# Kernel tuning notes

Hardware: AMD Instinct MI355X
Metric: run time of the kernel (lower is better)

## Reference

```python
import jax, jax.numpy as jnp
import numpy as np

EXP_CLAMP = 1.0e6
DENOM_EPS = 1e-10
LRELU_ALPHA = 0.01


def setup_inputs() -> dict:
    key = jax.random.key(0)
    k1, k2, k3, k4, k5, k6 = jax.random.split(key, 6)
    B, N, E, F = 4, 16384, 262144, 64
    h = jax.random.normal(k1, (B, N, F), dtype=jnp.float32)
    edge = jax.random.randint(k2, (B, E, 2), 0, N, dtype=jnp.int32)
    edge_num = jax.random.randint(k3, (B,), 1, E, dtype=jnp.int32)
    edge_weight = jax.random.uniform(k4, (B, E), dtype=jnp.float32)
    W = jax.random.normal(k5, (F, F), dtype=jnp.float32) * 0.15  # xavier-ish scale
    a = jax.random.normal(k6, (1, 2 * F), dtype=jnp.float32) * 0.12
    return {"h": h, "edge": edge, "edge_num": edge_num,
            "edge_weight": edge_weight, "W": W, "a": a}


def _seg_sum(src, idx, num_segments):
    # src: [E, ...], idx: [E] -> [num_segments, ...]
    return jax.ops.segment_sum(src, idx, num_segments=num_segments)


def reference(h, edge, edge_num, edge_weight, W, a):
    B, N, Fin = h.shape
    E = edge.shape[1]
    # linear transform: Wh = h @ W^T  -> [B, N, Fout]
    Wh = jnp.einsum('bnf,of->bno', h, W)
    ctr = edge[:, :, 0]  # [B, E]
    nbr = edge[:, :, 1]  # [B, E]
    Wh_c = jnp.take_along_axis(Wh, ctr[:, :, None], axis=1)  # [B, E, Fout]
    Wh_n = jnp.take_along_axis(Wh, nbr[:, :, None], axis=1)  # [B, E, Fout]
    a_input = jnp.concatenate([Wh_c, Wh_n], axis=-1) * edge_weight[:, :, None]
    # attention logits: leakyrelu(a_input @ a^T), squeeze to [B, E]
    att1 = jax.nn.leaky_relu(jnp.einsum('bek,k->be', a_input, a[0]), LRELU_ALPHA)
    # per-batch valid-edge mask (edges beyond edge_num zeroed, as in torch loop)
    mask = (jnp.arange(E, dtype=jnp.int32)[None, :] < edge_num[:, None])
    x_exp = jnp.clip(jnp.exp(att1), 0.0, EXP_CLAMP) * mask.astype(att1.dtype)
    # segment softmax denominator over center nodes
    denom = DENOM_EPS + jax.vmap(_seg_sum, in_axes=(0, 0, None))(x_exp, ctr, N)  # [B, N]
    att = x_exp / jnp.take_along_axis(denom, ctr, axis=1)  # [B, E]
    # weighted neighbor aggregation via scatter-add on center index
    att_Wh = Wh_n * att[:, :, None]  # masked edges already have att == 0
    h_prime = jax.vmap(_seg_sum, in_axes=(0, 0, None))(att_Wh, ctr, N)  # [B, N, Fout]
    return jax.nn.relu(h_prime)
```

## Files before the change

kernel.cpp:

```cpp
#include <hip/hip_runtime.h>

#define BB 4
#define NN 16384
#define EE 262144
#define FF 64
#define ROWS (BB * NN)
#define CAP 64
#define CHUNKS 64
#define CHUNK_E (EE / CHUNKS)
#define TILE_R 256

typedef __bf16 bf16x8 __attribute__((ext_vector_type(8)));
typedef float  f32x4  __attribute__((ext_vector_type(4)));

__device__ __forceinline__ unsigned short f32_to_bf16(float f) {
    unsigned int u = __float_as_uint(f);
    u += 0x7FFFu + ((u >> 16) & 1u);
    return (unsigned short)(u >> 16);
}

__global__ __launch_bounds__(256) void mfma_kernel(
    const float* __restrict__ h, const float* __restrict__ W,
    const float* __restrict__ a,
    unsigned short* __restrict__ Wh,
    float* __restrict__ sc, float* __restrict__ sn)
{
    __shared__ float wc[FF], wn[FF];
    const int t = threadIdx.x;
    const int lane = t & 63;
    const int m = lane & 15;
    const int q = lane >> 4;

    if (t < 128) {
        const int f = t & 63;
        const float* av = a + (t >> 6) * FF;
        float s = 0.0f;
        #pragma unroll 8
        for (int o = 0; o < FF; ++o)
            s = fmaf(av[o], W[o * FF + f], s);
        (t < 64 ? wc : wn)[f] = s;
    }

    bf16x8 bfrag[4][2];
    #pragma unroll
    for (int nt = 0; nt < 4; ++nt) {
        const float* wr = W + (nt * 16 + m) * FF;
        #pragma unroll
        for (int kh = 0; kh < 2; ++kh) {
            const float4 v0 = *(const float4*)(wr + kh * 32 + q * 8);
            const float4 v1 = *(const float4*)(wr + kh * 32 + q * 8 + 4);
            bf16x8 b;
            b[0] = (__bf16)v0.x; b[1] = (__bf16)v0.y;
            b[2] = (__bf16)v0.z; b[3] = (__bf16)v0.w;
            b[4] = (__bf16)v1.x; b[5] = (__bf16)v1.y;
            b[6] = (__bf16)v1.z; b[7] = (__bf16)v1.w;
            bfrag[nt][kh] = b;
        }
    }

    __syncthreads();

    const int waveId = (blockIdx.x * 256 + t) >> 6;
    const int R0 = waveId * 16;
    const float* hr = h + (size_t)(R0 + m) * FF;
    bf16x8 af[2];
    float s1 = 0.0f, s2 = 0.0f;
    #pragma unroll
    for (int kh = 0; kh < 2; ++kh) {
        const float4 v0 = *(const float4*)(hr + kh * 32 + q * 8);
        const float4 v1 = *(const float4*)(hr + kh * 32 + q * 8 + 4);
        bf16x8 aa;
        aa[0] = (__bf16)v0.x; aa[1] = (__bf16)v0.y;
        aa[2] = (__bf16)v0.z; aa[3] = (__bf16)v0.w;
        aa[4] = (__bf16)v1.x; aa[5] = (__bf16)v1.y;
        aa[6] = (__bf16)v1.z; aa[7] = (__bf16)v1.w;
        af[kh] = aa;
        const int fb = kh * 32 + q * 8;
        const float4 c0 = *(const float4*)&wc[fb];
        const float4 c1 = *(const float4*)&wc[fb + 4];
        const float4 n0 = *(const float4*)&wn[fb];
        const float4 n1 = *(const float4*)&wn[fb + 4];
        s1 = fmaf(v0.x, c0.x, fmaf(v0.y, c0.y, fmaf(v0.z, c0.z, fmaf(v0.w, c0.w, s1))));
        s1 = fmaf(v1.x, c1.x, fmaf(v1.y, c1.y, fmaf(v1.z, c1.z, fmaf(v1.w, c1.w, s1))));
        s2 = fmaf(v0.x, n0.x, fmaf(v0.y, n0.y, fmaf(v0.z, n0.z, fmaf(v0.w, n0.w, s2))));
        s2 = fmaf(v1.x, n1.x, fmaf(v1.y, n1.y, fmaf(v1.z, n1.z, fmaf(v1.w, n1.w, s2))));
    }
    s1 += __shfl_xor(s1, 16); s2 += __shfl_xor(s2, 16);
    s1 += __shfl_xor(s1, 32); s2 += __shfl_xor(s2, 32);
    if (lane < 16) { sc[R0 + m] = s1; sn[R0 + m] = s2; }

    #pragma unroll
    for (int nt = 0; nt < 4; ++nt) {
        f32x4 acc = {0.f, 0.f, 0.f, 0.f};
        acc = __builtin_amdgcn_mfma_f32_16x16x32_bf16(af[0], bfrag[nt][0], acc, 0, 0, 0);
        acc = __builtin_amdgcn_mfma_f32_16x16x32_bf16(af[1], bfrag[nt][1], acc, 0, 0, 0);
        #pragma unroll
        for (int i = 0; i < 4; ++i)
            Wh[(size_t)(R0 + q * 4 + i) * FF + nt * 16 + m] = f32_to_bf16(acc[i]);
    }
}

__global__ __launch_bounds__(256) void hist_kernel(
    const int* __restrict__ edge, const int* __restrict__ edge_num,
    unsigned short* __restrict__ histG)
{
    __shared__ unsigned int hist[NN];
    const int g = blockIdx.x;
    const int b = g >> 6, c = g & (CHUNKS - 1);
    const int t = threadIdx.x;
    const int en = edge_num[b];
    const int e0 = c * CHUNK_E;
    if (e0 >= en) return;

    for (int r = t; r < NN; r += 256) hist[r] = 0u;
    __syncthreads();

    const int2* ep = (const int2*)edge + (size_t)b * EE + e0;
    const int nAct = min(en - e0, CHUNK_E);
    for (int j = t; j < nAct; j += 256)
        atomicAdd(&hist[ep[j].x], 1u);
    __syncthreads();

    ushort2* out2 = (ushort2*)(histG + (size_t)g * NN);
    for (int r2 = t; r2 < NN / 2; r2 += 256) {
        ushort2 v;
        v.x = (unsigned short)hist[2 * r2];
        v.y = (unsigned short)hist[2 * r2 + 1];
        out2[r2] = v;
    }
}

__global__ __launch_bounds__(256) void scan_kernel(
    const int* __restrict__ edge_num,
    unsigned short* __restrict__ histG, int* __restrict__ cnt)
{
    __shared__ unsigned short tile[CHUNKS][TILE_R];
    const int g = blockIdx.x;
    const int b = g >> 6, tl = g & 63;
    const int r0 = tl * TILE_R;
    const int t = threadIdx.x;
    const int en = edge_num[b];
    const int nact = min((en + CHUNK_E - 1) / CHUNK_E, CHUNKS);

    for (int c = 0; c < nact; ++c)
        tile[c][t] = histG[(size_t)(b * CHUNKS + c) * NN + r0 + t];
    __syncthreads();

    unsigned int acc = 0;
    for (int c = 0; c < nact; ++c) {
        const unsigned int v = tile[c][t];
        tile[c][t] = (unsigned short)(acc > 65535u ? 65535u : acc);
        acc += v;
    }
    cnt[b * NN + r0 + t] = (int)acc;

    for (int c = 0; c < nact; ++c)
        histG[(size_t)(b * CHUNKS + c) * NN + r0 + t] = tile[c][t];
}

__global__ __launch_bounds__(256) void scatter_kernel(
    const int* __restrict__ edge, const int* __restrict__ edge_num,
    const unsigned short* __restrict__ baseG,
    unsigned int* __restrict__ payload)
{
    __shared__ unsigned int slotA[NN];
    const int g = blockIdx.x;
    const int b = g >> 6, c = g & (CHUNKS - 1);
    const int t = threadIdx.x;
    const int en = edge_num[b];
    const int e0 = c * CHUNK_E;
    if (e0 >= en) return;

    const ushort2* b2 = (const ushort2*)(baseG + (size_t)(b * CHUNKS + c) * NN);
    for (int r2 = t; r2 < NN / 2; r2 += 256) {
        const ushort2 v = b2[r2];
        slotA[2 * r2]     = v.x;
        slotA[2 * r2 + 1] = v.y;
    }
    __syncthreads();

    const int2* ep = (const int2*)edge + (size_t)b * EE + e0;
    const int nAct = min(en - e0, CHUNK_E);
    unsigned int* payB = payload + (size_t)b * NN * CAP;

    for (int j = t; j < nAct; j += 256) {
        const int2 e2 = ep[j];
        const unsigned int slot = atomicAdd(&slotA[e2.x], 1u);
        const unsigned int eid  = (unsigned int)(e0 + j);
        if (slot < CAP)
            payB[(size_t)e2.x * CAP + slot] = (eid << 14) | (unsigned int)e2.y;
    }
}

__global__ __launch_bounds__(256) void gather_kernel(
    const int* __restrict__ cnt, const unsigned int* __restrict__ payload,
    const uint2* __restrict__ Wh2,
    const float* __restrict__ sc, const float* __restrict__ sn,
    const float* __restrict__ ew,
    float* __restrict__ out)
{
    const int bi = blockIdx.x;
    const int xcd = bi & 7;
    const int batch = xcd >> 1;
    const int within = ((bi >> 3) << 1) | (xcd & 1);
    const int rg = batch * 4096 + within;

    const int lane = threadIdx.x & 63;
    const int wave = threadIdx.x >> 6;
    const int row = rg * 4 + wave;
    const int grp = lane >> 4;
    const int gl  = lane & 15;
    const unsigned int* pl = payload + (size_t)row * CAP;
    const uint2* WhB = Wh2 + (size_t)batch * NN * 16;
    const float* snB = sn + batch * NN;
    const float* ewB = ew + (size_t)batch * EE;

    int deg = cnt[row];
    const unsigned int praw = pl[lane];
    const float scr = sc[row];
    if (deg > CAP) deg = CAP;

    const float s0 = ewB[praw >> 14] * (scr + snB[praw & 0x3FFFu]);
    const float s1 = s0 > 0.0f ? s0 : 0.01f * s0;
    const float xe = fminf(__expf(s1), 1000000.0f);
    const unsigned int p = (lane < deg)
        ? (((__float_as_uint(xe) + 0x2000u) & 0xFFFFC000u) | (praw & 0x3FFFu))
        : 0u;

    float a0 = 0.f, a1 = 0.f, a2 = 0.f, a3 = 0.f, dsum = 0.f;
    for (int jj = 0; jj < deg; jj += 16) {
        const unsigned int pv0 = __shfl(p, jj + grp);
        const unsigned int pv1 = __shfl(p, jj + grp + 4);
        const unsigned int pv2 = __shfl(p, jj + grp + 8);
        const unsigned int pv3 = __shfl(p, jj + grp + 12);
        const uint2 w0 = WhB[(size_t)(pv0 & 0x3FFFu) * 16 + gl];
        const uint2 w1 = WhB[(size_t)(pv1 & 0x3FFFu) * 16 + gl];
        const uint2 w2 = WhB[(size_t)(pv2 & 0x3FFFu) * 16 + gl];
        const uint2 w3 = WhB[(size_t)(pv3 & 0x3FFFu) * 16 + gl];
        const float xe0 = __uint_as_float(pv0 & 0xFFFFC000u);
        const float xe1 = __uint_as_float(pv1 & 0xFFFFC000u);
        const float xe2 = __uint_as_float(pv2 & 0xFFFFC000u);
        const float xe3 = __uint_as_float(pv3 & 0xFFFFC000u);
        a0 = fmaf(xe0, __uint_as_float(w0.x << 16),         a0);
        a1 = fmaf(xe0, __uint_as_float(w0.x & 0xFFFF0000u), a1);
        a2 = fmaf(xe0, __uint_as_float(w0.y << 16),         a2);
        a3 = fmaf(xe0, __uint_as_float(w0.y & 0xFFFF0000u), a3);
        a0 = fmaf(xe1, __uint_as_float(w1.x << 16),         a0);
        a1 = fmaf(xe1, __uint_as_float(w1.x & 0xFFFF0000u), a1);
        a2 = fmaf(xe1, __uint_as_float(w1.y << 16),         a2);
        a3 = fmaf(xe1, __uint_as_float(w1.y & 0xFFFF0000u), a3);
        a0 = fmaf(xe2, __uint_as_float(w2.x << 16),         a0);
        a1 = fmaf(xe2, __uint_as_float(w2.x & 0xFFFF0000u), a1);
        a2 = fmaf(xe2, __uint_as_float(w2.y << 16),         a2);
        a3 = fmaf(xe2, __uint_as_float(w2.y & 0xFFFF0000u), a3);
        a0 = fmaf(xe3, __uint_as_float(w3.x << 16),         a0);
        a1 = fmaf(xe3, __uint_as_float(w3.x & 0xFFFF0000u), a1);
        a2 = fmaf(xe3, __uint_as_float(w3.y << 16),         a2);
        a3 = fmaf(xe3, __uint_as_float(w3.y & 0xFFFF0000u), a3);
        dsum += (xe0 + xe1) + (xe2 + xe3);
    }
    a0 += __shfl_xor(a0, 16); a1 += __shfl_xor(a1, 16);
    a2 += __shfl_xor(a2, 16); a3 += __shfl_xor(a3, 16);
    dsum += __shfl_xor(dsum, 16);
    a0 += __shfl_xor(a0, 32); a1 += __shfl_xor(a1, 32);
    a2 += __shfl_xor(a2, 32); a3 += __shfl_xor(a3, 32);
    dsum += __shfl_xor(dsum, 32);

    if (grp == 0) {
        const float inv = 1.0f / (1e-10f + dsum);
        float4 o;
        o.x = fmaxf(a0 * inv, 0.0f);
        o.y = fmaxf(a1 * inv, 0.0f);
        o.z = fmaxf(a2 * inv, 0.0f);
        o.w = fmaxf(a3 * inv, 0.0f);
        ((float4*)out)[(size_t)row * 16 + gl] = o;
    }
}

extern "C" void kernel_launch(void* const* d_in, const int* in_sizes, int n_in,
                              void* d_out, int out_size, void* d_ws, size_t ws_size,
                              hipStream_t stream)
{
    const float* h        = (const float*)d_in[0];
    const int*   edge     = (const int*)  d_in[1];
    const int*   edge_num = (const int*)  d_in[2];
    const float* ew       = (const float*)d_in[3];
    const float* W        = (const float*)d_in[4];
    const float* a        = (const float*)d_in[5];
    float* out = (float*)d_out;

    unsigned short* Wh = (unsigned short*)d_ws;
    float* sc        = (float*)(Wh + (size_t)BB * NN * FF);
    float* sn        = sc + ROWS;
    int*   cnt       = (int*)(sn + ROWS);
    unsigned int* payload = (unsigned int*)(cnt + ROWS);
    unsigned short* histG = (unsigned short*)(payload + (size_t)ROWS * CAP);

    mfma_kernel<<<1024, 256, 0, stream>>>(h, W, a, Wh, sc, sn);

    hist_kernel<<<BB * CHUNKS, 256, 0, stream>>>(edge, edge_num, histG);

    scan_kernel<<<BB * (NN / TILE_R), 256, 0, stream>>>(edge_num, histG, cnt);

    scatter_kernel<<<BB * CHUNKS, 256, 0, stream>>>(edge, edge_num,
                                                    histG, payload);

    gather_kernel<<<ROWS / 4, 256, 0, stream>>>(cnt, payload,
                                                (const uint2*)Wh,
                                                sc, sn, ew, out);
}
```

Before: 141.2 us.

## Process four rows per wave in gather and widen hist/scatter blocks

The gather kernel now gives each 16-lane group its own center row, so one wave handles four rows instead of one. Logits are computed in 16-edge batches, and the next batch's payload is prefetched while the current one runs, which removes the cross-group reductions and the waste on low-degree rows. The grid shrinks to 4096 blocks. The hist and scatter kernels move to 1024-thread blocks so more threads share each chunk's LDS atomics, at the risk of more contention and lower occupancy.

```diff
diff --git a/kernel.cpp b/kernel.cpp
--- a/kernel.cpp
+++ b/kernel.cpp
@@ -100,7 +100,7 @@
     }
 }
 
-__global__ __launch_bounds__(256) void hist_kernel(
+__global__ __launch_bounds__(1024) void hist_kernel(
     const int* __restrict__ edge, const int* __restrict__ edge_num,
     unsigned short* __restrict__ histG)
 {
@@ -112,17 +112,17 @@
     const int e0 = c * CHUNK_E;
     if (e0 >= en) return;
 
-    for (int r = t; r < NN; r += 256) hist[r] = 0u;
+    for (int r = t; r < NN; r += 1024) hist[r] = 0u;
     __syncthreads();
 
     const int2* ep = (const int2*)edge + (size_t)b * EE + e0;
     const int nAct = min(en - e0, CHUNK_E);
-    for (int j = t; j < nAct; j += 256)
+    for (int j = t; j < nAct; j += 1024)
         atomicAdd(&hist[ep[j].x], 1u);
     __syncthreads();
 
     ushort2* out2 = (ushort2*)(histG + (size_t)g * NN);
-    for (int r2 = t; r2 < NN / 2; r2 += 256) {
+    for (int r2 = t; r2 < NN / 2; r2 += 1024) {
         ushort2 v;
         v.x = (unsigned short)hist[2 * r2];
         v.y = (unsigned short)hist[2 * r2 + 1];
@@ -158,7 +158,7 @@
         histG[(size_t)(b * CHUNKS + c) * NN + r0 + t] = tile[c][t];
 }
 
-__global__ __launch_bounds__(256) void scatter_kernel(
+__global__ __launch_bounds__(1024) void scatter_kernel(
     const int* __restrict__ edge, const int* __restrict__ edge_num,
     const unsigned short* __restrict__ baseG,
     unsigned int* __restrict__ payload)
@@ -172,7 +172,7 @@
     if (e0 >= en) return;
 
     const ushort2* b2 = (const ushort2*)(baseG + (size_t)(b * CHUNKS + c) * NN);
-    for (int r2 = t; r2 < NN / 2; r2 += 256) {
+    for (int r2 = t; r2 < NN / 2; r2 += 1024) {
         const ushort2 v = b2[r2];
         slotA[2 * r2]     = v.x;
         slotA[2 * r2 + 1] = v.y;
@@ -183,7 +183,7 @@
     const int nAct = min(en - e0, CHUNK_E);
     unsigned int* payB = payload + (size_t)b * NN * CAP;
 
-    for (int j = t; j < nAct; j += 256) {
+    for (int j = t; j < nAct; j += 1024) {
         const int2 e2 = ep[j];
         const unsigned int slot = atomicAdd(&slotA[e2.x], 1u);
         const unsigned int eid  = (unsigned int)(e0 + j);
@@ -203,78 +203,88 @@
     const int xcd = bi & 7;
     const int batch = xcd >> 1;
     const int within = ((bi >> 3) << 1) | (xcd & 1);
-    const int rg = batch * 4096 + within;
-
+    const int w = threadIdx.x >> 6;
     const int lane = threadIdx.x & 63;
-    const int wave = threadIdx.x >> 6;
-    const int row = rg * 4 + wave;
-    const int grp = lane >> 4;
-    const int gl  = lane & 15;
+    const int r = lane >> 4;
+    const int f = lane & 15;
+    const int gbase = lane & 48;
+    const int rq = within * 4 + w;
+    const int row = batch * NN + rq * 4 + r;
+
     const unsigned int* pl = payload + (size_t)row * CAP;
     const uint2* WhB = Wh2 + (size_t)batch * NN * 16;
     const float* snB = sn + batch * NN;
     const float* ewB = ew + (size_t)batch * EE;
 
     int deg = cnt[row];
-    const unsigned int praw = pl[lane];
+    unsigned int raw = pl[f];
     const float scr = sc[row];
     if (deg > CAP) deg = CAP;
 
-    const float s0 = ewB[praw >> 14] * (scr + snB[praw & 0x3FFFu]);
-    const float s1 = s0 > 0.0f ? s0 : 0.01f * s0;
-    const float xe = fminf(__expf(s1), 1000000.0f);
-    const unsigned int p = (lane < deg)
-        ? (((__float_as_uint(xe) + 0x2000u) & 0xFFFFC000u) | (praw & 0x3FFFu))
-        : 0u;
-
-    float a0 = 0.f, a1 = 0.f, a2 = 0.f, a3 = 0.f, dsum = 0.f;
-    for (int jj = 0; jj < deg; jj += 16) {
-        const unsigned int pv0 = __shfl(p, jj + grp);
-        const unsigned int pv1 = __shfl(p, jj + grp + 4);
-        const unsigned int pv2 = __shfl(p, jj + grp + 8);
-        const unsigned int pv3 = __shfl(p, jj + grp + 12);
-        const uint2 w0 = WhB[(size_t)(pv0 & 0x3FFFu) * 16 + gl];
-        const uint2 w1 = WhB[(size_t)(pv1 & 0x3FFFu) * 16 + gl];
-        const uint2 w2 = WhB[(size_t)(pv2 & 0x3FFFu) * 16 + gl];
-        const uint2 w3 = WhB[(size_t)(pv3 & 0x3FFFu) * 16 + gl];
-        const float xe0 = __uint_as_float(pv0 & 0xFFFFC000u);
-        const float xe1 = __uint_as_float(pv1 & 0xFFFFC000u);
-        const float xe2 = __uint_as_float(pv2 & 0xFFFFC000u);
-        const float xe3 = __uint_as_float(pv3 & 0xFFFFC000u);
-        a0 = fmaf(xe0, __uint_as_float(w0.x << 16),         a0);
-        a1 = fmaf(xe0, __uint_as_float(w0.x & 0xFFFF0000u), a1);
-        a2 = fmaf(xe0, __uint_as_float(w0.y << 16),         a2);
-        a3 = fmaf(xe0, __uint_as_float(w0.y & 0xFFFF0000u), a3);
-        a0 = fmaf(xe1, __uint_as_float(w1.x << 16),         a0);
-        a1 = fmaf(xe1, __uint_as_float(w1.x & 0xFFFF0000u), a1);
-        a2 = fmaf(xe1, __uint_as_float(w1.y << 16),         a2);
-        a3 = fmaf(xe1, __uint_as_float(w1.y & 0xFFFF0000u), a3);
-        a0 = fmaf(xe2, __uint_as_float(w2.x << 16),         a0);
-        a1 = fmaf(xe2, __uint_as_float(w2.x & 0xFFFF0000u), a1);
-        a2 = fmaf(xe2, __uint_as_float(w2.y << 16),         a2);
-        a3 = fmaf(xe2, __uint_as_float(w2.y & 0xFFFF0000u), a3);
-        a0 = fmaf(xe3, __uint_as_float(w3.x << 16),         a0);
-        a1 = fmaf(xe3, __uint_as_float(w3.x & 0xFFFF0000u), a1);
-        a2 = fmaf(xe3, __uint_as_float(w3.y << 16),         a2);
-        a3 = fmaf(xe3, __uint_as_float(w3.y & 0xFFFF0000u), a3);
-        dsum += (xe0 + xe1) + (xe2 + xe3);
-    }
-    a0 += __shfl_xor(a0, 16); a1 += __shfl_xor(a1, 16);
-    a2 += __shfl_xor(a2, 16); a3 += __shfl_xor(a3, 16);
-    dsum += __shfl_xor(dsum, 16);
-    a0 += __shfl_xor(a0, 32); a1 += __shfl_xor(a1, 32);
-    a2 += __shfl_xor(a2, 32); a3 += __shfl_xor(a3, 32);
-    dsum += __shfl_xor(dsum, 32);
-
-    if (grp == 0) {
-        const float inv = 1.0f / (1e-10f + dsum);
-        float4 o;
-        o.x = fmaxf(a0 * inv, 0.0f);
-        o.y = fmaxf(a1 * inv, 0.0f);
-        o.z = fmaxf(a2 * inv, 0.0f);
-        o.w = fmaxf(a3 * inv, 0.0f);
-        ((float4*)out)[(size_t)row * 16 + gl] = o;
-    }
+    int jmax = deg;
+    jmax = max(jmax, __shfl_xor(jmax, 16));
+    jmax = max(jmax, __shfl_xor(jmax, 32));
+
+    float a0 = 0.f, a1 = 0.f, a2 = 0.f, a3 = 0.f, pdsum = 0.f;
+
+    for (int base = 0; base < jmax; base += 16) {
+        unsigned int p = 0u;
+        if (base + f < deg) {
+            const float s0 = ewB[raw >> 14] * (scr + snB[raw & 0x3FFFu]);
+            const float s1v = s0 > 0.0f ? s0 : 0.01f * s0;
+            const float xe = fminf(__expf(s1v), 1000000.0f);
+            pdsum += xe;
+            p = ((__float_as_uint(xe) + 0x2000u) & 0xFFFFC000u) | (raw & 0x3FFFu);
+        }
+        unsigned int rawN = 0u;
+        if (base + 16 < jmax) rawN = pl[base + 16 + f];
+
+        const int lim = min(16, jmax - base);
+        for (int j4 = 0; j4 < lim; j4 += 4) {
+            const unsigned int pv0 = __shfl(p, gbase + j4 + 0);
+            const unsigned int pv1 = __shfl(p, gbase + j4 + 1);
+            const unsigned int pv2 = __shfl(p, gbase + j4 + 2);
+            const unsigned int pv3 = __shfl(p, gbase + j4 + 3);
+            const uint2 w0 = WhB[(size_t)(pv0 & 0x3FFFu) * 16 + f];
+            const uint2 w1 = WhB[(size_t)(pv1 & 0x3FFFu) * 16 + f];
+            const uint2 w2 = WhB[(size_t)(pv2 & 0x3FFFu) * 16 + f];
+            const uint2 w3 = WhB[(size_t)(pv3 & 0x3FFFu) * 16 + f];
+            const float xe0 = __uint_as_float(pv0 & 0xFFFFC000u);
+            const float xe1 = __uint_as_float(pv1 & 0xFFFFC000u);
+            const float xe2 = __uint_as_float(pv2 & 0xFFFFC000u);
+            const float xe3 = __uint_as_float(pv3 & 0xFFFFC000u);
+            a0 = fmaf(xe0, __uint_as_float(w0.x << 16),         a0);
+            a1 = fmaf(xe0, __uint_as_float(w0.x & 0xFFFF0000u), a1);
+            a2 = fmaf(xe0, __uint_as_float(w0.y << 16),         a2);
+            a3 = fmaf(xe0, __uint_as_float(w0.y & 0xFFFF0000u), a3);
+            a0 = fmaf(xe1, __uint_as_float(w1.x << 16),         a0);
+            a1 = fmaf(xe1, __uint_as_float(w1.x & 0xFFFF0000u), a1);
+            a2 = fmaf(xe1, __uint_as_float(w1.y << 16),         a2);
+            a3 = fmaf(xe1, __uint_as_float(w1.y & 0xFFFF0000u), a3);
+            a0 = fmaf(xe2, __uint_as_float(w2.x << 16),         a0);
+            a1 = fmaf(xe2, __uint_as_float(w2.x & 0xFFFF0000u), a1);
+            a2 = fmaf(xe2, __uint_as_float(w2.y << 16),         a2);
+            a3 = fmaf(xe2, __uint_as_float(w2.y & 0xFFFF0000u), a3);
+            a0 = fmaf(xe3, __uint_as_float(w3.x << 16),         a0);
+            a1 = fmaf(xe3, __uint_as_float(w3.x & 0xFFFF0000u), a1);
+            a2 = fmaf(xe3, __uint_as_float(w3.y << 16),         a2);
+            a3 = fmaf(xe3, __uint_as_float(w3.y & 0xFFFF0000u), a3);
+        }
+        raw = rawN;
+    }
+
+    pdsum += __shfl_xor(pdsum, 1);
+    pdsum += __shfl_xor(pdsum, 2);
+    pdsum += __shfl_xor(pdsum, 4);
+    pdsum += __shfl_xor(pdsum, 8);
+
+    const float inv = 1.0f / (1e-10f + pdsum);
+    float4 o;
+    o.x = fmaxf(a0 * inv, 0.0f);
+    o.y = fmaxf(a1 * inv, 0.0f);
+    o.z = fmaxf(a2 * inv, 0.0f);
+    o.w = fmaxf(a3 * inv, 0.0f);
+    ((float4*)out)[(size_t)row * 16 + f] = o;
 }
 
 extern "C" void kernel_launch(void* const* d_in, const int* in_sizes, int n_in,
@@ -298,14 +308,14 @@
 
     mfma_kernel<<<1024, 256, 0, stream>>>(h, W, a, Wh, sc, sn);
 
-    hist_kernel<<<BB * CHUNKS, 256, 0, stream>>>(edge, edge_num, histG);
+    hist_kernel<<<BB * CHUNKS, 1024, 0, stream>>>(edge, edge_num, histG);
 
     scan_kernel<<<BB * (NN / TILE_R), 256, 0, stream>>>(edge_num, histG, cnt);
 
-    scatter_kernel<<<BB * CHUNKS, 256, 0, stream>>>(edge, edge_num,
-                                                    histG, payload);
-
-    gather_kernel<<<ROWS / 4, 256, 0, stream>>>(cnt, payload,
-                                                (const uint2*)Wh,
-                                                sc, sn, ew, out);
-}
+    scatter_kernel<<<BB * CHUNKS, 1024, 0, stream>>>(edge, edge_num,
+                                                     histG, payload);
+
+    gather_kernel<<<4096, 256, 0, stream>>>(cnt, payload,
+                                            (const uint2*)Wh,
+                                            sc, sn, ew, out);
+}
```

After: 134.0 us. 5.1% less time.
